# Kernel tuning notes

Hardware: AMD Instinct MI355X
Metric: run time of the kernel (lower is better)

The kernel has to match this reference:

```python
import jax, jax.numpy as jnp
import numpy as np

N = 100_000  # nodes
E = 1_600_000  # edges (avg degree 16)


def _lin_init(key, fan_in, fan_out):
    kw, kb = jax.random.split(key)
    s = 1.0 / np.sqrt(fan_in)
    W = jax.random.uniform(kw, (fan_in, fan_out), minval=-s, maxval=s, dtype=jnp.float32)
    b = jax.random.uniform(kb, (fan_out,), minval=-s, maxval=s, dtype=jnp.float32)
    return W, b


def setup_inputs() -> dict:
    key = jax.random.key(0)
    ks = jax.random.split(key, 14)
    x = jax.random.normal(ks[0], (N, 13), dtype=jnp.float32)
    edge_index = jax.random.randint(ks[1], (2, E), 0, N, dtype=jnp.int32)
    inp = {"x": x, "edge_index": edge_index}
    # lin_query/lin_key/lin_value -> heads*out_channels; lin_skip -> out width
    specs = [("q1", 13, 192), ("k1", 13, 192), ("v1", 13, 192), ("s1", 13, 64),
             ("q2", 64, 192), ("k2", 64, 192), ("v2", 64, 192), ("s2", 64, 64),
             ("q3", 64, 10), ("k3", 64, 10), ("v3", 64, 10), ("s3", 64, 10)]
    for i, (nm, fi, fo) in enumerate(specs):
        W, b = _lin_init(ks[2 + i], fi, fo)
        inp[nm + "_w"] = W
        inp[nm + "_b"] = b
    return inp


def _tconv(x, src, dst, Wq, bq, Wk, bk, Wv, bv, Ws, bs, H, C, concat):
    """PyG TransformerConv (edge_attr=None, beta=False, root_weight=True, dropout off)."""
    q = (x @ Wq + bq).reshape(-1, H, C)[dst]  # [E,H,C] query at target i
    k = (x @ Wk + bk).reshape(-1, H, C)[src]  # [E,H,C] key at source j
    v = (x @ Wv + bv).reshape(-1, H, C)[src]  # [E,H,C] value at source j
    logits = (q * k).sum(-1) * (1.0 / np.sqrt(C))  # [E,H]
    # segment softmax over incoming edges of each target node
    m = jax.ops.segment_max(logits, dst, num_segments=N)
    m = jnp.where(jnp.isfinite(m), m, 0.0)  # empty segments -> -inf -> 0
    e = jnp.exp(logits - m[dst])
    denom = jax.ops.segment_sum(e, dst, num_segments=N)
    alpha = e / (denom[dst] + 1e-16)  # [E,H]
    agg = jax.ops.segment_sum(alpha[:, :, None] * v, dst, num_segments=N)  # [N,H,C]
    out = agg.reshape(-1, H * C) if concat else agg.mean(axis=1)
    return out + x @ Ws + bs  # root/skip connection


def reference(x, edge_index,
              q1_w, q1_b, k1_w, k1_b, v1_w, v1_b, s1_w, s1_b,
              q2_w, q2_b, k2_w, k2_b, v2_w, v2_b, s2_w, s2_b,
              q3_w, q3_b, k3_w, k3_b, v3_w, v3_b, s3_w, s3_b):
    src, dst = edge_index[0], edge_index[1]
    h = jax.nn.relu(_tconv(x, src, dst, q1_w, q1_b, k1_w, k1_b, v1_w, v1_b, s1_w, s1_b, 3, 64, False))
    y = jax.nn.relu(_tconv(h, src, dst, q2_w, q2_b, k2_w, k2_b, v2_w, v2_b, s2_w, s2_b, 3, 64, False))
    h = y + h
    out = _tconv(h, src, dst, q3_w, q3_b, k3_w, k3_b, v3_w, v3_b, s3_w, s3_b, 1, 10, True)
    return jax.nn.log_softmax(out, axis=1)
```

## Files before the change

### kernel.cpp

```cpp
#include <hip/hip_runtime.h>
#include <math.h>

typedef unsigned int u32;
typedef unsigned short u16;


__device__ __forceinline__ float bf2f(u16 u) {
  union { u32 i; float f; } c; c.i = ((u32)u) << 16; return c.f;
}
__device__ __forceinline__ u16 f2bf(float f) {
  union { float f; u32 i; } c; c.f = f;
  u32 u = c.i;
  u32 r = u + 0x7fffu + ((u >> 16) & 1u);
  return (u16)(r >> 16);
}

__global__ __launch_bounds__(256) void zero_i32_kernel(int* __restrict__ p, int n) {
  int i = blockIdx.x * blockDim.x + threadIdx.x;
  if (i < n) p[i] = 0;
}

__global__ __launch_bounds__(256) void deg_kernel(
    const int* __restrict__ dst, int* __restrict__ deg, int E) {
  int e = blockIdx.x * blockDim.x + threadIdx.x;
  if (e < E) atomicAdd(&deg[dst[e]], 1);
}

__global__ __launch_bounds__(1024) void scan1_kernel(
    const int* __restrict__ deg, int* __restrict__ excl,
    int* __restrict__ bsum, int n) {
  __shared__ int wsum[16];
  int tid = threadIdx.x;
  int i = blockIdx.x * 1024 + tid;
  int v = (i < n) ? deg[i] : 0;
  int lane = tid & 63, w = tid >> 6;
  int val = v;
#pragma unroll
  for (int off = 1; off < 64; off <<= 1) {
    int t = __shfl_up(val, off, 64);
    if (lane >= off) val += t;
  }
  if (lane == 63) wsum[w] = val;
  __syncthreads();
  if (tid < 16) {
    int xv = wsum[tid];
    int xs = xv;
#pragma unroll
    for (int off = 1; off < 16; off <<= 1) {
      int t = __shfl_up(xs, off, 16);
      if (tid >= off) xs += t;
    }
    wsum[tid] = xs - xv;
  }
  __syncthreads();
  int incl = val + wsum[w];
  if (i < n) excl[i] = incl - v;
  if (tid == 1023) bsum[blockIdx.x] = incl;
}

__global__ __launch_bounds__(1024) void scan2_kernel(int* __restrict__ bsum, int nb) {
  __shared__ int wsum[16];
  int tid = threadIdx.x;
  int v = (tid < nb) ? bsum[tid] : 0;
  int lane = tid & 63, w = tid >> 6;
  int val = v;
#pragma unroll
  for (int off = 1; off < 64; off <<= 1) {
    int t = __shfl_up(val, off, 64);
    if (lane >= off) val += t;
  }
  if (lane == 63) wsum[w] = val;
  __syncthreads();
  if (tid < 16) {
    int xv = wsum[tid];
    int xs = xv;
#pragma unroll
    for (int off = 1; off < 16; off <<= 1) {
      int t = __shfl_up(xs, off, 16);
      if (tid >= off) xs += t;
    }
    wsum[tid] = xs - xv;
  }
  __syncthreads();
  int incl = val + wsum[w];
  if (tid < nb) bsum[tid] = incl - v;
}

__global__ __launch_bounds__(256) void scan3_kernel(
    const int* __restrict__ excl, const int* __restrict__ bsum,
    int* __restrict__ rowptr, int* __restrict__ cursor, int n, int E) {
  int i = blockIdx.x * blockDim.x + threadIdx.x;
  if (i < n) {
    int r = excl[i] + bsum[i >> 10];
    rowptr[i] = r;
    cursor[i] = r;
  }
  if (i == n) rowptr[n] = E;
}

__global__ __launch_bounds__(256) void scatter_kernel(
    const int* __restrict__ src, const int* __restrict__ dst,
    int* __restrict__ cursor, int* __restrict__ csr_src, int E) {
  int e = blockIdx.x * blockDim.x + threadIdx.x;
  if (e < E) {
    int pos = atomicAdd(&cursor[dst[e]], 1);
    csr_src[pos] = src[e];
  }
}

template<int FI, bool XBF>
__global__ __launch_bounds__(256) void kv_proj_v2(
    const void* __restrict__ xin,
    const float* __restrict__ Wk, const float* __restrict__ bk,
    const float* __restrict__ Wv, const float* __restrict__ bv,
    u16* __restrict__ kv, int n_nodes) {
  __shared__ u16 Wlds[FI * 384];
  __shared__ float blds[384];
  int tid = threadIdx.x;
  for (int idx = tid; idx < FI * 384; idx += 256) {
    int i = idx / 384;
    int j = idx - i * 384;
    int c = j / 6;
    int r = j - c * 6;
    int which = r / 3;
    int h = r - which * 3;
    int o = h * 64 + c;
    float w = which ? Wv[i * 192 + o] : Wk[i * 192 + o];
    Wlds[idx] = f2bf(w);
  }
  for (int j = tid; j < 384; j += 256) {
    int c = j / 6;
    int r = j - c * 6;
    int which = r / 3;
    int h = r - which * 3;
    int o = h * 64 + c;
    blds[j] = which ? bv[o] : bk[o];
  }
  __syncthreads();
  int wv = tid >> 6, lane = tid & 63;
  float b0 = blds[lane * 6 + 0], b1 = blds[lane * 6 + 1], b2 = blds[lane * 6 + 2];
  float b3 = blds[lane * 6 + 3], b4 = blds[lane * 6 + 4], b5 = blds[lane * 6 + 5];
#pragma unroll
  for (int t = 0; t < 8; ++t) {
    int n = blockIdx.x * 32 + wv * 8 + t;
    if (n >= n_nodes) break;
    float a0 = b0, a1 = b1, a2 = b2, a3 = b3, a4 = b4, a5 = b5;
    const u16* xb = (const u16*)xin + (size_t)n * FI;
    const float* xf = (const float*)xin + (size_t)n * FI;
#pragma unroll
    for (int i = 0; i < FI; ++i) {
      float xi = XBF ? bf2f(xb[i]) : xf[i];
      const u32* wr = (const u32*)(Wlds + i * 384 + 6 * lane);
      u32 w01 = wr[0], w23 = wr[1], w45 = wr[2];
      a0 = fmaf(xi, bf2f((u16)w01), a0);
      a1 = fmaf(xi, bf2f((u16)(w01 >> 16)), a1);
      a2 = fmaf(xi, bf2f((u16)w23), a2);
      a3 = fmaf(xi, bf2f((u16)(w23 >> 16)), a3);
      a4 = fmaf(xi, bf2f((u16)w45), a4);
      a5 = fmaf(xi, bf2f((u16)(w45 >> 16)), a5);
    }
    u32* outp = (u32*)(kv + (size_t)n * 384) + 3 * lane;
    outp[0] = (u32)f2bf(a0) | ((u32)f2bf(a1) << 16);
    outp[1] = (u32)f2bf(a2) | ((u32)f2bf(a3) << 16);
    outp[2] = (u32)f2bf(a4) | ((u32)f2bf(a5) << 16);
  }
}

template<int FI, bool XBF>
__global__ __launch_bounds__(256) void attn_l12_kernel(
    const void* __restrict__ xin,
    const float* __restrict__ Wq, const float* __restrict__ bq,
    const float* __restrict__ Ws, const float* __restrict__ bs,
    const u16* __restrict__ kv,
    const int* __restrict__ rowptr, const int* __restrict__ csr_src,
    const u16* __restrict__ resid,
    u16* __restrict__ hout, int n_nodes) {
  int wid = (blockIdx.x * blockDim.x + threadIdx.x) >> 6;
  int lane = threadIdx.x & 63;
  if (wid >= n_nodes) return;
  float q0 = bq[lane], q1 = bq[64 + lane], q2 = bq[128 + lane];
  float sk = bs[lane];
  {
    const u16* xb = (const u16*)xin + (size_t)wid * FI;
    const float* xf = (const float*)xin + (size_t)wid * FI;
#pragma unroll 4
    for (int i = 0; i < FI; ++i) {
      float xi = XBF ? bf2f(xb[i]) : xf[i];
      q0 = fmaf(xi, Wq[i * 192 + lane], q0);
      q1 = fmaf(xi, Wq[i * 192 + 64 + lane], q1);
      q2 = fmaf(xi, Wq[i * 192 + 128 + lane], q2);
      sk = fmaf(xi, Ws[i * 64 + lane], sk);
    }
  }
  const float scale = 0.125f;
  q0 *= scale; q1 *= scale; q2 *= scale;
  float m0 = -INFINITY, m1 = -INFINITY, m2 = -INFINITY;
  float s0 = 0.f, s1 = 0.f, s2 = 0.f;
  float a0 = 0.f, a1 = 0.f, a2 = 0.f;
  int beg = rowptr[wid], end = rowptr[wid + 1];
  int e = beg;
  for (; e + 2 <= end; e += 2) {
    int sa = csr_src[e], sb = csr_src[e + 1];
    const u32* pa = (const u32*)(kv + (size_t)sa * 384) + lane * 3;
    const u32* pb = (const u32*)(kv + (size_t)sb * 384) + lane * 3;
    u32 aw0 = pa[0], aw1 = pa[1], aw2 = pa[2];
    u32 bw0 = pb[0], bw1 = pb[1], bw2 = pb[2];
    float ka0 = bf2f((u16)aw0), ka1 = bf2f((u16)(aw0 >> 16)), ka2 = bf2f((u16)aw1);
    float va0 = bf2f((u16)(aw1 >> 16)), va1 = bf2f((u16)aw2), va2 = bf2f((u16)(aw2 >> 16));
    float kb0 = bf2f((u16)bw0), kb1 = bf2f((u16)(bw0 >> 16)), kb2 = bf2f((u16)bw1);
    float vb0 = bf2f((u16)(bw1 >> 16)), vb1 = bf2f((u16)bw2), vb2 = bf2f((u16)(bw2 >> 16));
    float xa0 = q0 * ka0, xa1 = q1 * ka1, xa2 = q2 * ka2;
    float xb0 = q0 * kb0, xb1 = q1 * kb1, xb2 = q2 * kb2;
#pragma unroll
    for (int off = 32; off >= 1; off >>= 1) {
      xa0 += __shfl_xor(xa0, off, 64);
      xa1 += __shfl_xor(xa1, off, 64);
      xa2 += __shfl_xor(xa2, off, 64);
      xb0 += __shfl_xor(xb0, off, 64);
      xb1 += __shfl_xor(xb1, off, 64);
      xb2 += __shfl_xor(xb2, off, 64);
    }
    float nm, sc, wa, wb;
    nm = fmaxf(fmaxf(m0, xa0), xb0);
    sc = __expf(m0 - nm); wa = __expf(xa0 - nm); wb = __expf(xb0 - nm);
    s0 = s0 * sc + wa + wb; a0 = a0 * sc + wa * va0 + wb * vb0; m0 = nm;
    nm = fmaxf(fmaxf(m1, xa1), xb1);
    sc = __expf(m1 - nm); wa = __expf(xa1 - nm); wb = __expf(xb1 - nm);
    s1 = s1 * sc + wa + wb; a1 = a1 * sc + wa * va1 + wb * vb1; m1 = nm;
    nm = fmaxf(fmaxf(m2, xa2), xb2);
    sc = __expf(m2 - nm); wa = __expf(xa2 - nm); wb = __expf(xb2 - nm);
    s2 = s2 * sc + wa + wb; a2 = a2 * sc + wa * va2 + wb * vb2; m2 = nm;
  }
  if (e < end) {
    int sa = csr_src[e];
    const u32* pa = (const u32*)(kv + (size_t)sa * 384) + lane * 3;
    u32 aw0 = pa[0], aw1 = pa[1], aw2 = pa[2];
    float ka0 = bf2f((u16)aw0), ka1 = bf2f((u16)(aw0 >> 16)), ka2 = bf2f((u16)aw1);
    float va0 = bf2f((u16)(aw1 >> 16)), va1 = bf2f((u16)aw2), va2 = bf2f((u16)(aw2 >> 16));
    float xa0 = q0 * ka0, xa1 = q1 * ka1, xa2 = q2 * ka2;
#pragma unroll
    for (int off = 32; off >= 1; off >>= 1) {
      xa0 += __shfl_xor(xa0, off, 64);
      xa1 += __shfl_xor(xa1, off, 64);
      xa2 += __shfl_xor(xa2, off, 64);
    }
    float nm, sc, wa;
    nm = fmaxf(m0, xa0); sc = __expf(m0 - nm); wa = __expf(xa0 - nm);
    s0 = s0 * sc + wa; a0 = a0 * sc + wa * va0; m0 = nm;
    nm = fmaxf(m1, xa1); sc = __expf(m1 - nm); wa = __expf(xa1 - nm);
    s1 = s1 * sc + wa; a1 = a1 * sc + wa * va1; m1 = nm;
    nm = fmaxf(m2, xa2); sc = __expf(m2 - nm); wa = __expf(xa2 - nm);
    s2 = s2 * sc + wa; a2 = a2 * sc + wa * va2; m2 = nm;
  }
  float val = (a0 / (s0 + 1e-16f) + a1 / (s1 + 1e-16f) + a2 / (s2 + 1e-16f)) *
              (1.0f / 3.0f);
  val += sk;
  val = fmaxf(val, 0.0f);
  if (resid) val += bf2f(resid[(size_t)wid * 64 + lane]);
  hout[(size_t)wid * 64 + lane] = f2bf(val);
}

__global__ __launch_bounds__(256) void kv3_proj_kernel(
    const u16* __restrict__ h,
    const float* __restrict__ Wk, const float* __restrict__ bk,
    const float* __restrict__ Wv, const float* __restrict__ bv,
    float* __restrict__ kv3, int n_nodes) {
  int idx = blockIdx.x * blockDim.x + threadIdx.x;
  if (idx >= n_nodes * 20) return;
  int n = idx / 20;
  int r = idx - n * 20;
  int which = r / 10;
  int o = r - which * 10;
  const float* W = which ? Wv : Wk;
  float acc = (which ? bv : bk)[o];
  const u16* hr = h + (size_t)n * 64;
#pragma unroll
  for (int i = 0; i < 64; ++i) acc = fmaf(bf2f(hr[i]), W[i * 10 + o], acc);
  kv3[(size_t)n * 20 + which * 10 + o] = acc;
}

__global__ __launch_bounds__(256) void attn_l3_kernel(
    const u16* __restrict__ h,
    const float* __restrict__ Wq, const float* __restrict__ bq,
    const float* __restrict__ Ws, const float* __restrict__ bs,
    const float* __restrict__ kv3,
    const int* __restrict__ rowptr, const int* __restrict__ csr_src,
    float* __restrict__ out, int n_nodes) {
  int tid = blockIdx.x * blockDim.x + threadIdx.x;
  int wid = tid >> 6;
  int lane = threadIdx.x & 63;
  int grp = lane >> 4;
  int sub = lane & 15;
  int n = wid * 4 + grp;
  bool an = (n < n_nodes);
  bool ca = an && (sub < 10);
  float q = 0.f, sk = 0.f;
  if (ca) { q = bq[sub]; sk = bs[sub]; }
  if (an) {
    const u16* hr = h + (size_t)n * 64;
#pragma unroll 4
    for (int i = 0; i < 64; ++i) {
      float xi = bf2f(hr[i]);
      if (sub < 10) {
        q = fmaf(xi, Wq[i * 10 + sub], q);
        sk = fmaf(xi, Ws[i * 10 + sub], sk);
      }
    }
  }
  q *= 0.31622776601683794f;
  float m = -INFINITY, s = 0.f, a = 0.f;
  int beg = 0, end = 0;
  if (an) { beg = rowptr[n]; end = rowptr[n + 1]; }
  for (int e = beg; e < end; ++e) {
    int srcn = csr_src[e];
    float kk = (sub < 10) ? kv3[(size_t)srcn * 20 + sub] : 0.f;
    float vv = (sub < 10) ? kv3[(size_t)srcn * 20 + 10 + sub] : 0.f;
    float p = q * kk;
    p += __shfl_xor(p, 1, 64);
    p += __shfl_xor(p, 2, 64);
    p += __shfl_xor(p, 4, 64);
    p += __shfl_xor(p, 8, 64);
    float nm = fmaxf(m, p);
    float sc = __expf(m - nm);
    float w = __expf(p - nm);
    s = s * sc + w;
    a = a * sc + w * vv;
    m = nm;
  }
  float z = 0.f;
  if (ca) z = a / (s + 1e-16f) + sk;
  float zm = (sub < 10) ? z : -INFINITY;
  float t;
  t = __shfl_xor(zm, 1, 64); zm = fmaxf(zm, t);
  t = __shfl_xor(zm, 2, 64); zm = fmaxf(zm, t);
  t = __shfl_xor(zm, 4, 64); zm = fmaxf(zm, t);
  t = __shfl_xor(zm, 8, 64); zm = fmaxf(zm, t);
  float ez = (sub < 10) ? __expf(z - zm) : 0.f;
  float se = ez;
  se += __shfl_xor(se, 1, 64);
  se += __shfl_xor(se, 2, 64);
  se += __shfl_xor(se, 4, 64);
  se += __shfl_xor(se, 8, 64);
  float ls = logf(se);
  if (ca) out[(size_t)n * 10 + sub] = (z - zm) - ls;
}

extern "C" void kernel_launch(void* const* d_in, const int* in_sizes, int n_in,
                              void* d_out, int out_size, void* d_ws, size_t ws_size,
                              hipStream_t stream) {
  const float* x = (const float*)d_in[0];
  const int* ei = (const int*)d_in[1];
  const int N = in_sizes[0] / 13;
  const int E = in_sizes[1] / 2;
  const int* esrc = ei;
  const int* edst = ei + E;

  const float* q1w = (const float*)d_in[2];  const float* q1b = (const float*)d_in[3];
  const float* k1w = (const float*)d_in[4];  const float* k1b = (const float*)d_in[5];
  const float* v1w = (const float*)d_in[6];  const float* v1b = (const float*)d_in[7];
  const float* s1w = (const float*)d_in[8];  const float* s1b = (const float*)d_in[9];
  const float* q2w = (const float*)d_in[10]; const float* q2b = (const float*)d_in[11];
  const float* k2w = (const float*)d_in[12]; const float* k2b = (const float*)d_in[13];
  const float* v2w = (const float*)d_in[14]; const float* v2b = (const float*)d_in[15];
  const float* s2w = (const float*)d_in[16]; const float* s2b = (const float*)d_in[17];
  const float* q3w = (const float*)d_in[18]; const float* q3b = (const float*)d_in[19];
  const float* k3w = (const float*)d_in[20]; const float* k3b = (const float*)d_in[21];
  const float* v3w = (const float*)d_in[22]; const float* v3b = (const float*)d_in[23];
  const float* s3w = (const float*)d_in[24]; const float* s3b = (const float*)d_in[25];

  size_t off = 0;
  auto carve = [&](size_t bytes) {
    void* p = (char*)d_ws + off;
    off += (bytes + 255) & ~(size_t)255;
    return p;
  };
  int* deg    = (int*)carve((size_t)N * 4);
  int* excl   = (int*)carve((size_t)N * 4);
  int* bsum   = (int*)carve(4096);
  int* rowptr = (int*)carve((size_t)(N + 1) * 4);
  int* cursor = (int*)carve((size_t)N * 4);
  int* csr    = (int*)carve((size_t)E * 4);
  u16* h1     = (u16*)carve((size_t)N * 64 * 2);
  u16* h2     = (u16*)carve((size_t)N * 64 * 2);
  float* kv3  = (float*)carve((size_t)N * 20 * 4);
  u16* kv     = (u16*)carve((size_t)N * 384 * 2);
  if (off > ws_size) return;

  int nb = (N + 1023) / 1024;
  zero_i32_kernel<<<(N + 255) / 256, 256, 0, stream>>>(deg, N);
  deg_kernel<<<(E + 255) / 256, 256, 0, stream>>>(edst, deg, E);
  scan1_kernel<<<nb, 1024, 0, stream>>>(deg, excl, bsum, N);
  scan2_kernel<<<1, 1024, 0, stream>>>(bsum, nb);
  scan3_kernel<<<(N + 1 + 255) / 256, 256, 0, stream>>>(excl, bsum, rowptr, cursor, N, E);
  scatter_kernel<<<(E + 255) / 256, 256, 0, stream>>>(esrc, edst, cursor, csr, E);

  int attn_blocks = (N + 3) / 4;
  int proj_blocks = (N + 31) / 32;
  kv_proj_v2<13, false><<<proj_blocks, 256, 0, stream>>>(
      x, k1w, k1b, v1w, v1b, kv, N);
  attn_l12_kernel<13, false><<<attn_blocks, 256, 0, stream>>>(
      x, q1w, q1b, s1w, s1b, kv, rowptr, csr, nullptr, h1, N);
  kv_proj_v2<64, true><<<proj_blocks, 256, 0, stream>>>(
      h1, k2w, k2b, v2w, v2b, kv, N);
  attn_l12_kernel<64, true><<<attn_blocks, 256, 0, stream>>>(
      h1, q2w, q2b, s2w, s2b, kv, rowptr, csr, h1, h2, N);
  kv3_proj_kernel<<<(N * 20 + 255) / 256, 256, 0, stream>>>(
      h2, k3w, k3b, v3w, v3b, kv3, N);
  attn_l3_kernel<<<(N + 15) / 16, 256, 0, stream>>>(
      h2, q3w, q3b, s3w, s3b, kv3, rowptr, csr, (float*)d_out, N);
}
```

Measured before the change: 1.384 ms.

## Regroup KV layout so 16-lane groups process separate edges with vector loads

Reorders the packed K/V row so each lane's 4 channels across all heads sit in 48 contiguous bytes. The attention kernel now splits each wave into four 16-lane groups that each handle two edges, with one online softmax per group merged at the end. Each lane loads its data with 128-bit vector loads and the shuffle reduction shrinks from 6 to 4 steps. The aim is to cut shuffle overhead and raise memory-level parallelism on the gather, at the cost of extra merge work, padding waste on low-degree nodes, and only a quarter of the lanes storing the output.

```diff
diff --git a/kernel.cpp b/kernel.cpp
--- a/kernel.cpp
+++ b/kernel.cpp
@@ -13,6 +13,12 @@
   u32 u = c.i;
   u32 r = u + 0x7fffu + ((u >> 16) & 1u);
   return (u16)(r >> 16);
+}
+__device__ __forceinline__ float blo(u32 w) {
+  union { u32 i; float f; } c; c.i = w << 16; return c.f;
+}
+__device__ __forceinline__ float bhi(u32 w) {
+  union { u32 i; float f; } c; c.i = w & 0xffff0000u; return c.f;
 }
 
 __global__ __launch_bounds__(256) void zero_i32_kernel(int* __restrict__ p, int n) {
@@ -119,22 +125,26 @@
   int tid = threadIdx.x;
   for (int idx = tid; idx < FI * 384; idx += 256) {
     int i = idx / 384;
-    int j = idx - i * 384;
-    int c = j / 6;
-    int r = j - c * 6;
-    int which = r / 3;
-    int h = r - which * 3;
-    int o = h * 64 + c;
+    int s = idx - i * 384;
+    int g = s / 24;
+    int r = s - g * 24;
+    int which = r / 12;
+    int rr = r - which * 12;
+    int h = rr >> 2;
+    int cs = rr & 3;
+    int o = h * 64 + (g * 4 + cs);
     float w = which ? Wv[i * 192 + o] : Wk[i * 192 + o];
     Wlds[idx] = f2bf(w);
   }
-  for (int j = tid; j < 384; j += 256) {
-    int c = j / 6;
-    int r = j - c * 6;
-    int which = r / 3;
-    int h = r - which * 3;
-    int o = h * 64 + c;
-    blds[j] = which ? bv[o] : bk[o];
+  for (int s = tid; s < 384; s += 256) {
+    int g = s / 24;
+    int r = s - g * 24;
+    int which = r / 12;
+    int rr = r - which * 12;
+    int h = rr >> 2;
+    int cs = rr & 3;
+    int o = h * 64 + (g * 4 + cs);
+    blds[s] = which ? bv[o] : bk[o];
   }
   __syncthreads();
   int wv = tid >> 6, lane = tid & 63;
@@ -152,12 +162,12 @@
       float xi = XBF ? bf2f(xb[i]) : xf[i];
       const u32* wr = (const u32*)(Wlds + i * 384 + 6 * lane);
       u32 w01 = wr[0], w23 = wr[1], w45 = wr[2];
-      a0 = fmaf(xi, bf2f((u16)w01), a0);
-      a1 = fmaf(xi, bf2f((u16)(w01 >> 16)), a1);
-      a2 = fmaf(xi, bf2f((u16)w23), a2);
-      a3 = fmaf(xi, bf2f((u16)(w23 >> 16)), a3);
-      a4 = fmaf(xi, bf2f((u16)w45), a4);
-      a5 = fmaf(xi, bf2f((u16)(w45 >> 16)), a5);
+      a0 = fmaf(xi, blo(w01), a0);
+      a1 = fmaf(xi, bhi(w01), a1);
+      a2 = fmaf(xi, blo(w23), a2);
+      a3 = fmaf(xi, bhi(w23), a3);
+      a4 = fmaf(xi, blo(w45), a4);
+      a5 = fmaf(xi, bhi(w45), a5);
     }
     u32* outp = (u32*)(kv + (size_t)n * 384) + 3 * lane;
     outp[0] = (u32)f2bf(a0) | ((u32)f2bf(a1) << 16);
@@ -167,7 +177,7 @@
 }
 
 template<int FI, bool XBF>
-__global__ __launch_bounds__(256) void attn_l12_kernel(
+__global__ __launch_bounds__(256) void attn_l12_v3(
     const void* __restrict__ xin,
     const float* __restrict__ Wq, const float* __restrict__ bq,
     const float* __restrict__ Ws, const float* __restrict__ bs,
@@ -194,70 +204,111 @@
   }
   const float scale = 0.125f;
   q0 *= scale; q1 *= scale; q2 *= scale;
-  float m0 = -INFINITY, m1 = -INFINITY, m2 = -INFINITY;
-  float s0 = 0.f, s1 = 0.f, s2 = 0.f;
-  float a0 = 0.f, a1 = 0.f, a2 = 0.f;
+  int glane = lane & 15;
+  int grp = lane >> 4;
+  float qp[3][4], skp[4];
+#pragma unroll
+  for (int cs = 0; cs < 4; ++cs) {
+    int srcl = 4 * glane + cs;
+    qp[0][cs] = __shfl(q0, srcl, 64);
+    qp[1][cs] = __shfl(q1, srcl, 64);
+    qp[2][cs] = __shfl(q2, srcl, 64);
+    skp[cs] = __shfl(sk, srcl, 64);
+  }
+  float m[3] = {-1e30f, -1e30f, -1e30f};
+  float sden[3] = {0.f, 0.f, 0.f};
+  float acc[3][4] = {{0.f, 0.f, 0.f, 0.f}, {0.f, 0.f, 0.f, 0.f}, {0.f, 0.f, 0.f, 0.f}};
   int beg = rowptr[wid], end = rowptr[wid + 1];
-  int e = beg;
-  for (; e + 2 <= end; e += 2) {
-    int sa = csr_src[e], sb = csr_src[e + 1];
-    const u32* pa = (const u32*)(kv + (size_t)sa * 384) + lane * 3;
-    const u32* pb = (const u32*)(kv + (size_t)sb * 384) + lane * 3;
-    u32 aw0 = pa[0], aw1 = pa[1], aw2 = pa[2];
-    u32 bw0 = pb[0], bw1 = pb[1], bw2 = pb[2];
-    float ka0 = bf2f((u16)aw0), ka1 = bf2f((u16)(aw0 >> 16)), ka2 = bf2f((u16)aw1);
-    float va0 = bf2f((u16)(aw1 >> 16)), va1 = bf2f((u16)aw2), va2 = bf2f((u16)(aw2 >> 16));
-    float kb0 = bf2f((u16)bw0), kb1 = bf2f((u16)(bw0 >> 16)), kb2 = bf2f((u16)bw1);
-    float vb0 = bf2f((u16)(bw1 >> 16)), vb1 = bf2f((u16)bw2), vb2 = bf2f((u16)(bw2 >> 16));
-    float xa0 = q0 * ka0, xa1 = q1 * ka1, xa2 = q2 * ka2;
-    float xb0 = q0 * kb0, xb1 = q1 * kb1, xb2 = q2 * kb2;
-#pragma unroll
-    for (int off = 32; off >= 1; off >>= 1) {
-      xa0 += __shfl_xor(xa0, off, 64);
-      xa1 += __shfl_xor(xa1, off, 64);
-      xa2 += __shfl_xor(xa2, off, 64);
-      xb0 += __shfl_xor(xb0, off, 64);
-      xb1 += __shfl_xor(xb1, off, 64);
-      xb2 += __shfl_xor(xb2, off, 64);
-    }
-    float nm, sc, wa, wb;
-    nm = fmaxf(fmaxf(m0, xa0), xb0);
-    sc = __expf(m0 - nm); wa = __expf(xa0 - nm); wb = __expf(xb0 - nm);
-    s0 = s0 * sc + wa + wb; a0 = a0 * sc + wa * va0 + wb * vb0; m0 = nm;
-    nm = fmaxf(fmaxf(m1, xa1), xb1);
-    sc = __expf(m1 - nm); wa = __expf(xa1 - nm); wb = __expf(xb1 - nm);
-    s1 = s1 * sc + wa + wb; a1 = a1 * sc + wa * va1 + wb * vb1; m1 = nm;
-    nm = fmaxf(fmaxf(m2, xa2), xb2);
-    sc = __expf(m2 - nm); wa = __expf(xa2 - nm); wb = __expf(xb2 - nm);
-    s2 = s2 * sc + wa + wb; a2 = a2 * sc + wa * va2 + wb * vb2; m2 = nm;
-  }
-  if (e < end) {
-    int sa = csr_src[e];
-    const u32* pa = (const u32*)(kv + (size_t)sa * 384) + lane * 3;
-    u32 aw0 = pa[0], aw1 = pa[1], aw2 = pa[2];
-    float ka0 = bf2f((u16)aw0), ka1 = bf2f((u16)(aw0 >> 16)), ka2 = bf2f((u16)aw1);
-    float va0 = bf2f((u16)(aw1 >> 16)), va1 = bf2f((u16)aw2), va2 = bf2f((u16)(aw2 >> 16));
-    float xa0 = q0 * ka0, xa1 = q1 * ka1, xa2 = q2 * ka2;
-#pragma unroll
-    for (int off = 32; off >= 1; off >>= 1) {
-      xa0 += __shfl_xor(xa0, off, 64);
-      xa1 += __shfl_xor(xa1, off, 64);
-      xa2 += __shfl_xor(xa2, off, 64);
-    }
-    float nm, sc, wa;
-    nm = fmaxf(m0, xa0); sc = __expf(m0 - nm); wa = __expf(xa0 - nm);
-    s0 = s0 * sc + wa; a0 = a0 * sc + wa * va0; m0 = nm;
-    nm = fmaxf(m1, xa1); sc = __expf(m1 - nm); wa = __expf(xa1 - nm);
-    s1 = s1 * sc + wa; a1 = a1 * sc + wa * va1; m1 = nm;
-    nm = fmaxf(m2, xa2); sc = __expf(m2 - nm); wa = __expf(xa2 - nm);
-    s2 = s2 * sc + wa; a2 = a2 * sc + wa * va2; m2 = nm;
-  }
-  float val = (a0 / (s0 + 1e-16f) + a1 / (s1 + 1e-16f) + a2 / (s2 + 1e-16f)) *
-              (1.0f / 3.0f);
-  val += sk;
-  val = fmaxf(val, 0.0f);
-  if (resid) val += bf2f(resid[(size_t)wid * 64 + lane]);
-  hout[(size_t)wid * 64 + lane] = f2bf(val);
+  int el = end - 1;
+  for (int base = beg; base < end; base += 8) {
+    int e0 = base + grp * 2;
+    int e1 = e0 + 1;
+    bool v0 = e0 < end, v1 = e1 < end;
+    int sa = csr_src[v0 ? e0 : el];
+    int sb = csr_src[v1 ? e1 : el];
+    const uint4* pa = (const uint4*)(kv + (size_t)sa * 384 + glane * 24);
+    const uint4* pb = (const uint4*)(kv + (size_t)sb * 384 + glane * 24);
+    uint4 A0 = pa[0], A1 = pa[1], A2 = pa[2];
+    uint4 B0 = pb[0], B1 = pb[1], B2 = pb[2];
+    float dA[3], dB[3];
+#pragma unroll
+    for (int h = 0; h < 3; ++h) {
+      u32 ka0 = (h == 0) ? A0.x : (h == 1) ? A0.z : A1.x;
+      u32 ka1 = (h == 0) ? A0.y : (h == 1) ? A0.w : A1.y;
+      u32 kb0 = (h == 0) ? B0.x : (h == 1) ? B0.z : B1.x;
+      u32 kb1 = (h == 0) ? B0.y : (h == 1) ? B0.w : B1.y;
+      dA[h] = fmaf(qp[h][0], blo(ka0), fmaf(qp[h][1], bhi(ka0),
+              fmaf(qp[h][2], blo(ka1), qp[h][3] * bhi(ka1))));
+      dB[h] = fmaf(qp[h][0], blo(kb0), fmaf(qp[h][1], bhi(kb0),
+              fmaf(qp[h][2], blo(kb1), qp[h][3] * bhi(kb1))));
+    }
+#pragma unroll
+    for (int off = 1; off <= 8; off <<= 1) {
+#pragma unroll
+      for (int h = 0; h < 3; ++h) {
+        dA[h] += __shfl_xor(dA[h], off, 64);
+        dB[h] += __shfl_xor(dB[h], off, 64);
+      }
+    }
+#pragma unroll
+    for (int h = 0; h < 3; ++h) {
+      float pa_ = v0 ? dA[h] : -1e30f;
+      float pb_ = v1 ? dB[h] : -1e30f;
+      float nm = fmaxf(m[h], fmaxf(pa_, pb_));
+      float sc = __expf(m[h] - nm);
+      float wa = v0 ? __expf(pa_ - nm) : 0.f;
+      float wb = v1 ? __expf(pb_ - nm) : 0.f;
+      sden[h] = sden[h] * sc + wa + wb;
+      u32 va0 = (h == 0) ? A1.z : (h == 1) ? A2.x : A2.z;
+      u32 va1 = (h == 0) ? A1.w : (h == 1) ? A2.y : A2.w;
+      u32 vb0 = (h == 0) ? B1.z : (h == 1) ? B2.x : B2.z;
+      u32 vb1 = (h == 0) ? B1.w : (h == 1) ? B2.y : B2.w;
+      acc[h][0] = fmaf(acc[h][0], sc, fmaf(wa, blo(va0), wb * blo(vb0)));
+      acc[h][1] = fmaf(acc[h][1], sc, fmaf(wa, bhi(va0), wb * bhi(vb0)));
+      acc[h][2] = fmaf(acc[h][2], sc, fmaf(wa, blo(va1), wb * blo(vb1)));
+      acc[h][3] = fmaf(acc[h][3], sc, fmaf(wa, bhi(va1), wb * bhi(vb1)));
+      m[h] = nm;
+    }
+  }
+#pragma unroll
+  for (int off = 16; off <= 32; off <<= 1) {
+#pragma unroll
+    for (int h = 0; h < 3; ++h) {
+      float mo = __shfl_xor(m[h], off, 64);
+      float so = __shfl_xor(sden[h], off, 64);
+      float nm = fmaxf(m[h], mo);
+      float c1 = __expf(m[h] - nm);
+      float c2 = __expf(mo - nm);
+      sden[h] = sden[h] * c1 + so * c2;
+#pragma unroll
+      for (int cs = 0; cs < 4; ++cs) {
+        float ao = __shfl_xor(acc[h][cs], off, 64);
+        acc[h][cs] = acc[h][cs] * c1 + ao * c2;
+      }
+      m[h] = nm;
+    }
+  }
+  if (grp == 0) {
+    float r0 = 1.f / (sden[0] + 1e-16f);
+    float r1 = 1.f / (sden[1] + 1e-16f);
+    float r2 = 1.f / (sden[2] + 1e-16f);
+    float o_[4];
+#pragma unroll
+    for (int cs = 0; cs < 4; ++cs) {
+      float val = (acc[0][cs] * r0 + acc[1][cs] * r1 + acc[2][cs] * r2) * (1.0f / 3.0f);
+      val += skp[cs];
+      o_[cs] = fmaxf(val, 0.0f);
+    }
+    if (resid) {
+      uint2 rr = *(const uint2*)(resid + (size_t)wid * 64 + glane * 4);
+      o_[0] += blo(rr.x); o_[1] += bhi(rr.x);
+      o_[2] += blo(rr.y); o_[3] += bhi(rr.y);
+    }
+    uint2 pack;
+    pack.x = (u32)f2bf(o_[0]) | ((u32)f2bf(o_[1]) << 16);
+    pack.y = (u32)f2bf(o_[2]) | ((u32)f2bf(o_[3]) << 16);
+    *(uint2*)(hout + (size_t)wid * 64 + glane * 4) = pack;
+  }
 }
 
 __global__ __launch_bounds__(256) void kv3_proj_kernel(
@@ -398,11 +449,11 @@
   int proj_blocks = (N + 31) / 32;
   kv_proj_v2<13, false><<<proj_blocks, 256, 0, stream>>>(
       x, k1w, k1b, v1w, v1b, kv, N);
-  attn_l12_kernel<13, false><<<attn_blocks, 256, 0, stream>>>(
+  attn_l12_v3<13, false><<<attn_blocks, 256, 0, stream>>>(
       x, q1w, q1b, s1w, s1b, kv, rowptr, csr, nullptr, h1, N);
   kv_proj_v2<64, true><<<proj_blocks, 256, 0, stream>>>(
       h1, k2w, k2b, v2w, v2b, kv, N);
-  attn_l12_kernel<64, true><<<attn_blocks, 256, 0, stream>>>(
+  attn_l12_v3<64, true><<<attn_blocks, 256, 0, stream>>>(
       h1, q2w, q2b, s2w, s2b, kv, rowptr, csr, h1, h2, N);
   kv3_proj_kernel<<<(N * 20 + 255) / 256, 256, 0, stream>>>(
       h2, k3w, k3b, v3w, v3b, kv3, N);
```

Result: faster. 1.299 ms (-6.1%).
